# Optimization experiments

Measured on AMD Instinct MI355X. Metric: run time of the kernel, lower is better.

## Reference

```python
import jax, jax.numpy as jnp
import numpy as np

N_LAYERS = 2
D_MODEL = 1024
D_INNER = 2 * D_MODEL
D_STATE = 16
D_CONV = 4
DT_RANK = D_MODEL // 16  # 64
B_SZ, L = 1, 2048
EPS = 1e-5


def layernorm(x, w, b):
    mu = jnp.mean(x, axis=-1, keepdims=True)
    var = jnp.mean(jnp.square(x - mu), axis=-1, keepdims=True)
    return (x - mu) * jax.lax.rsqrt(var + EPS) * w + b


def mamba(x, in_w, cw, cb, xp_w, dtp_w, dtp_b, A_log, Dp, out_w):
    # x: [B, L, D_MODEL]
    Bn, Ln, _ = x.shape
    xz = jnp.einsum('bld,ed->ble', x, in_w)          # [B,L,2*D_INNER]
    xc, z = jnp.split(xz, 2, axis=-1)
    # causal depthwise conv1d (kernel D_CONV)
    xp = jnp.pad(xc, ((0, 0), (D_CONV - 1, 0), (0, 0)))
    xc = sum(xp[:, k:k + Ln, :] * cw[:, k] for k in range(D_CONV)) + cb
    xc = jax.nn.silu(xc)
    dbl = jnp.einsum('ble,re->blr', xc, xp_w)        # [B,L,DT_RANK+2*D_STATE]
    dt, Bm, Cm = jnp.split(dbl, [DT_RANK, DT_RANK + D_STATE], axis=-1)
    dt = jax.nn.softplus(jnp.einsum('blr,er->ble', dt, dtp_w) + dtp_b)  # [B,L,E]
    A = -jnp.exp(A_log)                              # [E,N], strictly negative
    dA = jnp.exp(dt[..., None] * A)                  # [B,L,E,N]
    dBu = (dt * xc)[..., None] * Bm[:, :, None, :]   # [B,L,E,N]

    def step(h, inp):
        dA_t, dBu_t, C_t = inp
        h = dA_t * h + dBu_t                         # [B,E,N]
        y = jnp.einsum('ben,bn->be', h, C_t)
        return h, y

    h0 = jnp.zeros((Bn, D_INNER, D_STATE), dA.dtype)
    _, ys = jax.lax.scan(step, h0, (dA.transpose(1, 0, 2, 3),
                                    dBu.transpose(1, 0, 2, 3),
                                    Cm.transpose(1, 0, 2)))
    y = ys.transpose(1, 0, 2) + xc * Dp              # [B,L,E]
    y = y * jax.nn.silu(z)
    return jnp.einsum('ble,de->bld', y, out_w)       # [B,L,D_MODEL]


def setup_inputs() -> dict:
    key = jax.random.key(0)
    ks = jax.random.split(key, 12)
    s = 0.02
    dt_init = np.log(np.expm1(0.01)).astype(np.float32)  # softplus^-1(0.01)
    A_row = jnp.log(jnp.arange(1, D_STATE + 1, dtype=jnp.float32))
    return {
        'x': jax.random.normal(ks[0], (B_SZ, L, D_MODEL), jnp.float32),
        'ln_w': jnp.ones((N_LAYERS, D_MODEL), jnp.float32),
        'ln_b': jnp.zeros((N_LAYERS, D_MODEL), jnp.float32),
        'in_proj_w': jax.random.normal(ks[1], (N_LAYERS, 2 * D_INNER, D_MODEL)) * s,
        'conv_w': jax.random.normal(ks[2], (N_LAYERS, D_INNER, D_CONV)) * 0.2,
        'conv_b': jnp.zeros((N_LAYERS, D_INNER), jnp.float32),
        'x_proj_w': jax.random.normal(ks[3], (N_LAYERS, DT_RANK + 2 * D_STATE, D_INNER)) * s,
        'dt_proj_w': jax.random.normal(ks[4], (N_LAYERS, D_INNER, DT_RANK)) * (DT_RANK ** -0.5),
        'dt_proj_b': jnp.full((N_LAYERS, D_INNER), dt_init),
        'A_log': jnp.broadcast_to(A_row, (N_LAYERS, D_INNER, D_STATE)).copy(),
        'D_skip': jnp.ones((N_LAYERS, D_INNER), jnp.float32),
        'out_proj_w': jax.random.normal(ks[5], (N_LAYERS, D_MODEL, D_INNER)) * s,
        'norm_f_w': jnp.ones((D_MODEL,), jnp.float32),
        'norm_f_b': jnp.zeros((D_MODEL,), jnp.float32),
    }


def reference(x, ln_w, ln_b, in_proj_w, conv_w, conv_b, x_proj_w, dt_proj_w,
              dt_proj_b, A_log, D_skip, out_proj_w, norm_f_w, norm_f_b):
    for i in range(N_LAYERS):
        h = layernorm(x, ln_w[i], ln_b[i])
        h = mamba(h, in_proj_w[i], conv_w[i], conv_b[i], x_proj_w[i],
                  dt_proj_w[i], dt_proj_b[i], A_log[i], D_skip[i], out_proj_w[i])
        x = h + x  # residual (dropout/drop_path are identity in eval)
    return layernorm(x, norm_f_w, norm_f_b)
```

## Files before the change

### kernel.cpp

```cpp
#include <hip/hip_runtime.h>
#include <hip/hip_bf16.h>
#include <math.h>

#define LSEQ 2048
#define DMODEL 1024
#define DINNER 2048
#define DSTATE 16
#define DCONV 4
#define DTRANK 64
#define RPROJ 96

#define CHUNK 32
#define NCHUNK (LSEQ / CHUNK)

typedef __attribute__((ext_vector_type(8))) short bf16x8;
typedef __attribute__((ext_vector_type(4))) float f32x4;

__device__ __forceinline__ float softplusf(float x) {
    return (x > 20.f) ? x : log1pf(__expf(x));
}
__device__ __forceinline__ float siluf(float x) {
    return x / (1.f + __expf(-x));
}
__device__ __forceinline__ short f2bf(float f) {
    union { float f; unsigned u; } v; v.f = f;
    unsigned r = v.u + 0x7FFFu + ((v.u >> 16) & 1u);
    return (short)(r >> 16);
}

__global__ __launch_bounds__(256) void cvt_bf16(
    const float* __restrict__ s, short* __restrict__ d, int n)
{
    const int i = (blockIdx.x * 256 + threadIdx.x) * 8;
    if (i >= n) return;
    const float4 a = *(const float4*)(s + i);
    const float4 b = *(const float4*)(s + i + 4);
    alignas(16) short h[8];
    h[0] = f2bf(a.x); h[1] = f2bf(a.y); h[2] = f2bf(a.z); h[3] = f2bf(a.w);
    h[4] = f2bf(b.x); h[5] = f2bf(b.y); h[6] = f2bf(b.z); h[7] = f2bf(b.w);
    *(uint4*)(d + i) = *(const uint4*)h;
}

__global__ __launch_bounds__(256) void ln_kernel(
    const float* __restrict__ x, const float* __restrict__ w,
    const float* __restrict__ b, float* __restrict__ outf,
    short* __restrict__ outb)
{
    __shared__ float s1[256], s2[256];
    const int row = blockIdx.x;
    const int tid = threadIdx.x;
    const float* xr = x + (size_t)row * DMODEL;
    float v[4];
    float s = 0.f, sq = 0.f;
#pragma unroll
    for (int k = 0; k < 4; k++) {
        v[k] = xr[k * 256 + tid];
        s += v[k];
        sq += v[k] * v[k];
    }
    s1[tid] = s; s2[tid] = sq;
    __syncthreads();
    for (int off = 128; off > 0; off >>= 1) {
        if (tid < off) { s1[tid] += s1[tid + off]; s2[tid] += s2[tid + off]; }
        __syncthreads();
    }
    const float mu = s1[0] * (1.f / DMODEL);
    const float var = s2[0] * (1.f / DMODEL) - mu * mu;
    const float rstd = rsqrtf(var + 1e-5f);
#pragma unroll
    for (int k = 0; k < 4; k++) {
        const int i = k * 256 + tid;
        const float o = (v[k] - mu) * rstd * w[i] + b[i];
        if (outf) outf[(size_t)row * DMODEL + i] = o;
        if (outb) outb[(size_t)row * DMODEL + i] = f2bf(o);
    }
}

template<int BN_T, int MODE>
__global__ __launch_bounds__(256) void gemm_mfma(
    const short* __restrict__ A,
    const short* __restrict__ W,
    float* __restrict__ C, int ldc,
    int M, int N, int K,
    const float* __restrict__ resid)
{
    constexpr int BK = 32;
    constexpr int HN = BN_T / 2;
    constexpr int NJ = BN_T / 32;
    constexpr int WISS = (BN_T * BK * 2) / 4096;
    __shared__ alignas(16) short As[128 * BK];
    __shared__ alignas(16) short Ws[BN_T * BK];

    const int tid = threadIdx.x;
    const int lane = tid & 63;
    const int w = tid >> 6;
    const int wr = w >> 1, wc = w & 1;
    const int row0 = blockIdx.y * 128;
    const int col0 = blockIdx.x * BN_T;

    const int srow = tid >> 2;
    const int skch = (tid & 3) * 8;

    f32x4 acc[4][NJ];
#pragma unroll
    for (int i = 0; i < 4; i++)
#pragma unroll
        for (int j = 0; j < NJ; j++) acc[i][j] = (f32x4)0.f;

    const int lrow = lane & 15;
    const int lk = (lane >> 4) * 8;

    for (int kt = 0; kt < K; kt += BK) {
        __syncthreads();
#pragma unroll
        for (int j = 0; j < 2; j++) {
            const short* gp = A + (size_t)(row0 + j * 64 + srow) * K + kt + skch;
            short* lp = As + j * 2048 + w * 512;
            __builtin_amdgcn_global_load_lds(
                (const __attribute__((address_space(1))) void*)gp,
                (__attribute__((address_space(3))) void*)lp, 16, 0, 0);
        }
#pragma unroll
        for (int j = 0; j < WISS; j++) {
            const int wrow = col0 + j * 64 + srow;
            const short* gp = W + (size_t)wrow * K + kt + skch;
            short* lp = Ws + j * 2048 + w * 512;
            if (wrow < N)
                __builtin_amdgcn_global_load_lds(
                    (const __attribute__((address_space(1))) void*)gp,
                    (__attribute__((address_space(3))) void*)lp, 16, 0, 0);
        }
        __syncthreads();

        bf16x8 af[4], bfr[NJ];
#pragma unroll
        for (int i = 0; i < 4; i++)
            af[i] = *(const bf16x8*)&As[(wr * 64 + i * 16 + lrow) * BK + lk];
#pragma unroll
        for (int j = 0; j < NJ; j++)
            bfr[j] = *(const bf16x8*)&Ws[(wc * HN + j * 16 + lrow) * BK + lk];
#pragma unroll
        for (int i = 0; i < 4; i++)
#pragma unroll
            for (int j = 0; j < NJ; j++)
                acc[i][j] = __builtin_amdgcn_mfma_f32_16x16x32_bf16(
                    af[i], bfr[j], acc[i][j], 0, 0, 0);
    }

    const int rbase = row0 + wr * 64;
    const int cbase = col0 + wc * HN;
#pragma unroll
    for (int i = 0; i < 4; i++) {
#pragma unroll
        for (int j = 0; j < NJ; j++) {
            const int gcol = cbase + j * 16 + lrow;
            if (gcol < N) {
#pragma unroll
                for (int r = 0; r < 4; r++) {
                    const int grow = rbase + i * 16 + (lane >> 4) * 4 + r;
                    float v = acc[i][j][r];
                    if (MODE == 2) v += resid[(size_t)grow * ldc + gcol];
                    C[(size_t)grow * ldc + gcol] = v;
                }
            }
        }
    }
}

#define BM 64
#define BN 64
#define BK16 16
__global__ __launch_bounds__(256) void gemm_nt(
    const float* __restrict__ A, int lda,
    const float* __restrict__ W, int ldw,
    float* __restrict__ C, int ldc,
    int M, int N, int K,
    const float* __restrict__ bias)
{
    __shared__ float As[BK16][BM];
    __shared__ float Ws[BK16][BN];
    const int tid = threadIdx.x;
    const int row0 = blockIdx.y * BM;
    const int col0 = blockIdx.x * BN;
    const int lr = tid >> 2;
    const int lk = (tid & 3) << 2;
    const int tx = tid & 15;
    const int ty = tid >> 4;

    float acc[4][4] = {{0.f}};

    for (int kt = 0; kt < K; kt += BK16) {
        const float4 av = *(const float4*)(A + (size_t)(row0 + lr) * lda + kt + lk);
        As[lk + 0][lr] = av.x; As[lk + 1][lr] = av.y;
        As[lk + 2][lr] = av.z; As[lk + 3][lr] = av.w;
        const float4 wv = *(const float4*)(W + (size_t)(col0 + lr) * ldw + kt + lk);
        Ws[lk + 0][lr] = wv.x; Ws[lk + 1][lr] = wv.y;
        Ws[lk + 2][lr] = wv.z; Ws[lk + 3][lr] = wv.w;
        __syncthreads();
#pragma unroll
        for (int k = 0; k < BK16; k++) {
            const float4 a4 = *(const float4*)&As[k][ty * 4];
            const float4 w4 = *(const float4*)&Ws[k][tx * 4];
            acc[0][0] += a4.x * w4.x; acc[0][1] += a4.x * w4.y;
            acc[0][2] += a4.x * w4.z; acc[0][3] += a4.x * w4.w;
            acc[1][0] += a4.y * w4.x; acc[1][1] += a4.y * w4.y;
            acc[1][2] += a4.y * w4.z; acc[1][3] += a4.y * w4.w;
            acc[2][0] += a4.z * w4.x; acc[2][1] += a4.z * w4.y;
            acc[2][2] += a4.z * w4.z; acc[2][3] += a4.z * w4.w;
            acc[3][0] += a4.w * w4.x; acc[3][1] += a4.w * w4.y;
            acc[3][2] += a4.w * w4.z; acc[3][3] += a4.w * w4.w;
        }
        __syncthreads();
    }

    const int c = col0 + tx * 4;
#pragma unroll
    for (int i = 0; i < 4; i++) {
        const int r = row0 + ty * 4 + i;
        float4 v = make_float4(acc[i][0], acc[i][1], acc[i][2], acc[i][3]);
        v.x = softplusf(v.x + bias[c + 0]);
        v.y = softplusf(v.y + bias[c + 1]);
        v.z = softplusf(v.z + bias[c + 2]);
        v.w = softplusf(v.w + bias[c + 3]);
        *(float4*)(C + (size_t)r * ldc + c) = v;
    }
}

__global__ __launch_bounds__(256) void conv_silu_kernel(
    const float* __restrict__ xz, const float* __restrict__ cw,
    const float* __restrict__ cb, float* __restrict__ xc,
    short* __restrict__ xcb)
{
    const int g = blockIdx.x * 256 + threadIdx.x;
    const int c = g & (DINNER - 1);
    const int t = g >> 11;
    float acc = cb[c];
#pragma unroll
    for (int k = 0; k < DCONV; k++) {
        const int tt = t - (DCONV - 1) + k;
        if (tt >= 0) acc += xz[(size_t)tt * (2 * DINNER) + c] * cw[c * DCONV + k];
    }
    const float o = siluf(acc);
    xc[(size_t)t * DINNER + c] = o;
    xcb[(size_t)t * DINNER + c] = f2bf(o);
}

__global__ __launch_bounds__(256) void scan_pass1(
    const float* __restrict__ dt,
    const float* __restrict__ xc,
    const float* __restrict__ dbl,
    const float* __restrict__ A_log,
    float* __restrict__ S,
    float* __restrict__ sumdt)
{
    const int e = blockIdx.x * 256 + threadIdx.x;
    const int c = blockIdx.y;
    float a[DSTATE];
#pragma unroll
    for (int n = 0; n < DSTATE; n++) a[n] = -__expf(A_log[(size_t)e * DSTATE + n]);
    float h[DSTATE];
#pragma unroll
    for (int n = 0; n < DSTATE; n++) h[n] = 0.f;
    float sd = 0.f;

    __shared__ float sBC[CHUNK][32];
    for (int i = threadIdx.x; i < CHUNK * 32; i += 256) {
        const int tl = i >> 5, j = i & 31;
        sBC[tl][j] = dbl[(size_t)(c * CHUNK + tl) * RPROJ + DTRANK + j];
    }
    __syncthreads();

    for (int tl = 0; tl < CHUNK; tl++) {
        const int t = c * CHUNK + tl;
        const float dtv = dt[(size_t)t * DINNER + e];
        const float du = dtv * xc[(size_t)t * DINNER + e];
        sd += dtv;
#pragma unroll
        for (int n = 0; n < DSTATE; n++) {
            const float dA = __expf(dtv * a[n]);
            h[n] = dA * h[n] + du * sBC[tl][n];
        }
    }
    sumdt[(size_t)c * DINNER + e] = sd;
#pragma unroll
    for (int n = 0; n < DSTATE; n++)
        S[((size_t)c * DSTATE + n) * DINNER + e] = h[n];
}

__global__ __launch_bounds__(256) void scan_pass2(
    const float* __restrict__ A_log,
    const float* __restrict__ sumdt,
    float* __restrict__ S)
{
    const int idx = blockIdx.x * 256 + threadIdx.x;
    const int e = idx & (DINNER - 1);
    const int n = idx >> 11;
    const float a = -__expf(A_log[(size_t)e * DSTATE + n]);
    float H = 0.f;
    for (int c = 0; c < NCHUNK; c++) {
        const size_t off = ((size_t)c * DSTATE + n) * DINNER + e;
        const float tmp = S[off];
        S[off] = H;
        const float P = __expf(a * sumdt[(size_t)c * DINNER + e]);
        H = P * H + tmp;
    }
}

__global__ __launch_bounds__(256) void scan_pass3(
    const float* __restrict__ dt,
    const float* __restrict__ xc,
    const float* __restrict__ dbl,
    const float* __restrict__ xz,
    const float* __restrict__ A_log,
    const float* __restrict__ Dp,
    const float* __restrict__ S,
    short* __restrict__ yb)
{
    const int e = blockIdx.x * 256 + threadIdx.x;
    const int c = blockIdx.y;
    float a[DSTATE];
#pragma unroll
    for (int n = 0; n < DSTATE; n++) a[n] = -__expf(A_log[(size_t)e * DSTATE + n]);
    float h[DSTATE];
#pragma unroll
    for (int n = 0; n < DSTATE; n++)
        h[n] = S[((size_t)c * DSTATE + n) * DINNER + e];
    const float dskip = Dp[e];

    __shared__ float sBC[CHUNK][32];
    for (int i = threadIdx.x; i < CHUNK * 32; i += 256) {
        const int tl = i >> 5, j = i & 31;
        sBC[tl][j] = dbl[(size_t)(c * CHUNK + tl) * RPROJ + DTRANK + j];
    }
    __syncthreads();

    for (int tl = 0; tl < CHUNK; tl++) {
        const int t = c * CHUNK + tl;
        const float dtv = dt[(size_t)t * DINNER + e];
        const float xcv = xc[(size_t)t * DINNER + e];
        const float du = dtv * xcv;
        float yv = 0.f;
#pragma unroll
        for (int n = 0; n < DSTATE; n++) {
            const float dA = __expf(dtv * a[n]);
            h[n] = dA * h[n] + du * sBC[tl][n];
            yv += h[n] * sBC[tl][16 + n];
        }
        const float zv = xz[(size_t)t * (2 * DINNER) + DINNER + e];
        yv = (yv + xcv * dskip) * siluf(zv);
        yb[(size_t)t * DINNER + e] = f2bf(yv);
    }
}

extern "C" void kernel_launch(void* const* d_in, const int* in_sizes, int n_in,
                              void* d_out, int out_size, void* d_ws, size_t ws_size,
                              hipStream_t stream) {
    const float* x_in   = (const float*)d_in[0];
    const float* ln_w   = (const float*)d_in[1];
    const float* ln_b   = (const float*)d_in[2];
    const float* in_w   = (const float*)d_in[3];
    const float* conv_w = (const float*)d_in[4];
    const float* conv_b = (const float*)d_in[5];
    const float* xp_w   = (const float*)d_in[6];
    const float* dtp_w  = (const float*)d_in[7];
    const float* dtp_b  = (const float*)d_in[8];
    const float* A_log  = (const float*)d_in[9];
    const float* D_skip = (const float*)d_in[10];
    const float* out_w  = (const float*)d_in[11];
    const float* nf_w   = (const float*)d_in[12];
    const float* nf_b   = (const float*)d_in[13];
    float* out = (float*)d_out;

    float* w = (float*)d_ws;
    float* buf_x = w; w += (size_t)LSEQ * DMODEL;
    float* xz    = w; w += (size_t)LSEQ * 2 * DINNER;
    float* xc    = w; w += (size_t)LSEQ * DINNER;
    float* dbl   = w; w += (size_t)LSEQ * RPROJ;
    float* dtb   = w; w += (size_t)LSEQ * DINNER;
    float* Sbuf  = w; w += (size_t)NCHUNK * DSTATE * DINNER;
    float* sumdt = w; w += (size_t)NCHUNK * DINNER;
    short* h_bf    = (short*)w; w += (size_t)LSEQ * DMODEL / 2;
    short* xc_bf   = (short*)w; w += (size_t)LSEQ * DINNER / 2;
    short* y_bf    = (short*)w; w += (size_t)LSEQ * DINNER / 2;
    short* in_w_bf  = (short*)w; w += (size_t)2 * (2 * DINNER) * DMODEL / 2;
    short* xp_w_bf  = (short*)w; w += (size_t)2 * RPROJ * DINNER / 2;
    short* out_w_bf = (short*)w; w += (size_t)2 * DMODEL * DINNER / 2;

    {
        const int n1 = 2 * (2 * DINNER) * DMODEL;
        cvt_bf16<<<dim3(n1 / (256 * 8)), dim3(256), 0, stream>>>(in_w, in_w_bf, n1);
        const int n2 = 2 * RPROJ * DINNER;
        cvt_bf16<<<dim3(n2 / (256 * 8)), dim3(256), 0, stream>>>(xp_w, xp_w_bf, n2);
        const int n3 = 2 * DMODEL * DINNER;
        cvt_bf16<<<dim3(n3 / (256 * 8)), dim3(256), 0, stream>>>(out_w, out_w_bf, n3);
    }

    for (int layer = 0; layer < 2; layer++) {
        const float* resid_src = (layer == 0) ? x_in : buf_x;
        ln_kernel<<<dim3(LSEQ), dim3(256), 0, stream>>>(
            resid_src, ln_w + layer * DMODEL, ln_b + layer * DMODEL,
            nullptr, h_bf);
        gemm_mfma<128, 0><<<dim3((2 * DINNER) / 128, LSEQ / 128), dim3(256), 0, stream>>>(
            h_bf, in_w_bf + (size_t)layer * 2 * DINNER * DMODEL,
            xz, 2 * DINNER, LSEQ, 2 * DINNER, DMODEL, nullptr);
        conv_silu_kernel<<<dim3((LSEQ * DINNER) / 256), dim3(256), 0, stream>>>(
            xz, conv_w + (size_t)layer * DINNER * DCONV, conv_b + layer * DINNER,
            xc, xc_bf);
        gemm_mfma<64, 0><<<dim3((RPROJ + 63) / 64, LSEQ / 128), dim3(256), 0, stream>>>(
            xc_bf, xp_w_bf + (size_t)layer * RPROJ * DINNER,
            dbl, RPROJ, LSEQ, RPROJ, DINNER, nullptr);
        gemm_nt<<<dim3(DINNER / BN, LSEQ / BM), dim3(256), 0, stream>>>(
            dbl, RPROJ, dtp_w + (size_t)layer * DINNER * DTRANK, DTRANK,
            dtb, DINNER, LSEQ, DINNER, DTRANK, dtp_b + layer * DINNER);
        const float* Al = A_log + (size_t)layer * DINNER * DSTATE;
        scan_pass1<<<dim3(DINNER / 256, NCHUNK), dim3(256), 0, stream>>>(
            dtb, xc, dbl, Al, Sbuf, sumdt);
        scan_pass2<<<dim3((DINNER * DSTATE) / 256), dim3(256), 0, stream>>>(
            Al, sumdt, Sbuf);
        scan_pass3<<<dim3(DINNER / 256, NCHUNK), dim3(256), 0, stream>>>(
            dtb, xc, dbl, xz, Al, D_skip + layer * DINNER, Sbuf, y_bf);
        gemm_mfma<64, 2><<<dim3(DMODEL / 64, LSEQ / 128), dim3(256), 0, stream>>>(
            y_bf, out_w_bf + (size_t)layer * DMODEL * DINNER,
            buf_x, DMODEL, LSEQ, DMODEL, DINNER, resid_src);
    }
    ln_kernel<<<dim3(LSEQ), dim3(256), 0, stream>>>(buf_x, nf_w, nf_b, out, nullptr);
}
```

Before: 530.1 us.

## Store xz and xc intermediates in bf16 and run dt_proj on MFMA

The in_proj GEMM now writes its output directly as bf16, and the fp32 xc buffer is removed. Conv, scan_pass1 and scan_pass3 read bf16 xz and xc and widen them to fp32. The fp32 SIMT dt_proj GEMM is replaced by the bf16 MFMA GEMM, which applies the fused bias and softplus in its epilogue, fed by a bf16 copy of dbl and dt_proj weights. The goal is to cut memory traffic on the large intermediates and speed up the dt projection, at the cost of reduced precision in dt, xc and z.

```diff
diff --git a/kernel.cpp b/kernel.cpp
--- a/kernel.cpp
+++ b/kernel.cpp
@@ -26,6 +26,11 @@
     union { float f; unsigned u; } v; v.f = f;
     unsigned r = v.u + 0x7FFFu + ((v.u >> 16) & 1u);
     return (short)(r >> 16);
+}
+__device__ __forceinline__ float bf2f(short h) {
+    union { unsigned u; float f; } v;
+    v.u = ((unsigned)(unsigned short)h) << 16;
+    return v.f;
 }
 
 __global__ __launch_bounds__(256) void cvt_bf16(
@@ -78,10 +83,11 @@
 
 template<int BN_T, int MODE>
 __global__ __launch_bounds__(256) void gemm_mfma(
-    const short* __restrict__ A,
-    const short* __restrict__ W,
-    float* __restrict__ C, int ldc,
+    const short* __restrict__ A, int lda,
+    const short* __restrict__ W, int ldw,
+    float* __restrict__ Cf, short* __restrict__ Cb, int ldc,
     int M, int N, int K,
+    const float* __restrict__ bias,
     const float* __restrict__ resid)
 {
     constexpr int BK = 32;
@@ -114,7 +120,7 @@
         __syncthreads();
 #pragma unroll
         for (int j = 0; j < 2; j++) {
-            const short* gp = A + (size_t)(row0 + j * 64 + srow) * K + kt + skch;
+            const short* gp = A + (size_t)(row0 + j * 64 + srow) * lda + kt + skch;
             short* lp = As + j * 2048 + w * 512;
             __builtin_amdgcn_global_load_lds(
                 (const __attribute__((address_space(1))) void*)gp,
@@ -123,7 +129,7 @@
 #pragma unroll
         for (int j = 0; j < WISS; j++) {
             const int wrow = col0 + j * 64 + srow;
-            const short* gp = W + (size_t)wrow * K + kt + skch;
+            const short* gp = W + (size_t)wrow * ldw + kt + skch;
             short* lp = Ws + j * 2048 + w * 512;
             if (wrow < N)
                 __builtin_amdgcn_global_load_lds(
@@ -159,77 +165,23 @@
                 for (int r = 0; r < 4; r++) {
                     const int grow = rbase + i * 16 + (lane >> 4) * 4 + r;
                     float v = acc[i][j][r];
+                    if (MODE == 1) v = softplusf(v + bias[gcol]);
                     if (MODE == 2) v += resid[(size_t)grow * ldc + gcol];
-                    C[(size_t)grow * ldc + gcol] = v;
+                    if (MODE == 3) {
+                        Cb[(size_t)grow * ldc + gcol] = f2bf(v);
+                    } else {
+                        Cf[(size_t)grow * ldc + gcol] = v;
+                        if (MODE == 4) Cb[(size_t)grow * ldc + gcol] = f2bf(v);
+                    }
                 }
             }
         }
     }
 }
 
-#define BM 64
-#define BN 64
-#define BK16 16
-__global__ __launch_bounds__(256) void gemm_nt(
-    const float* __restrict__ A, int lda,
-    const float* __restrict__ W, int ldw,
-    float* __restrict__ C, int ldc,
-    int M, int N, int K,
-    const float* __restrict__ bias)
-{
-    __shared__ float As[BK16][BM];
-    __shared__ float Ws[BK16][BN];
-    const int tid = threadIdx.x;
-    const int row0 = blockIdx.y * BM;
-    const int col0 = blockIdx.x * BN;
-    const int lr = tid >> 2;
-    const int lk = (tid & 3) << 2;
-    const int tx = tid & 15;
-    const int ty = tid >> 4;
-
-    float acc[4][4] = {{0.f}};
-
-    for (int kt = 0; kt < K; kt += BK16) {
-        const float4 av = *(const float4*)(A + (size_t)(row0 + lr) * lda + kt + lk);
-        As[lk + 0][lr] = av.x; As[lk + 1][lr] = av.y;
-        As[lk + 2][lr] = av.z; As[lk + 3][lr] = av.w;
-        const float4 wv = *(const float4*)(W + (size_t)(col0 + lr) * ldw + kt + lk);
-        Ws[lk + 0][lr] = wv.x; Ws[lk + 1][lr] = wv.y;
-        Ws[lk + 2][lr] = wv.z; Ws[lk + 3][lr] = wv.w;
-        __syncthreads();
-#pragma unroll
-        for (int k = 0; k < BK16; k++) {
-            const float4 a4 = *(const float4*)&As[k][ty * 4];
-            const float4 w4 = *(const float4*)&Ws[k][tx * 4];
-            acc[0][0] += a4.x * w4.x; acc[0][1] += a4.x * w4.y;
-            acc[0][2] += a4.x * w4.z; acc[0][3] += a4.x * w4.w;
-            acc[1][0] += a4.y * w4.x; acc[1][1] += a4.y * w4.y;
-            acc[1][2] += a4.y * w4.z; acc[1][3] += a4.y * w4.w;
-            acc[2][0] += a4.z * w4.x; acc[2][1] += a4.z * w4.y;
-            acc[2][2] += a4.z * w4.z; acc[2][3] += a4.z * w4.w;
-            acc[3][0] += a4.w * w4.x; acc[3][1] += a4.w * w4.y;
-            acc[3][2] += a4.w * w4.z; acc[3][3] += a4.w * w4.w;
-        }
-        __syncthreads();
-    }
-
-    const int c = col0 + tx * 4;
-#pragma unroll
-    for (int i = 0; i < 4; i++) {
-        const int r = row0 + ty * 4 + i;
-        float4 v = make_float4(acc[i][0], acc[i][1], acc[i][2], acc[i][3]);
-        v.x = softplusf(v.x + bias[c + 0]);
-        v.y = softplusf(v.y + bias[c + 1]);
-        v.z = softplusf(v.z + bias[c + 2]);
-        v.w = softplusf(v.w + bias[c + 3]);
-        *(float4*)(C + (size_t)r * ldc + c) = v;
-    }
-}
-
 __global__ __launch_bounds__(256) void conv_silu_kernel(
-    const float* __restrict__ xz, const float* __restrict__ cw,
-    const float* __restrict__ cb, float* __restrict__ xc,
-    short* __restrict__ xcb)
+    const short* __restrict__ xzb, const float* __restrict__ cw,
+    const float* __restrict__ cb, short* __restrict__ xcb)
 {
     const int g = blockIdx.x * 256 + threadIdx.x;
     const int c = g & (DINNER - 1);
@@ -238,16 +190,15 @@
 #pragma unroll
     for (int k = 0; k < DCONV; k++) {
         const int tt = t - (DCONV - 1) + k;
-        if (tt >= 0) acc += xz[(size_t)tt * (2 * DINNER) + c] * cw[c * DCONV + k];
-    }
-    const float o = siluf(acc);
-    xc[(size_t)t * DINNER + c] = o;
-    xcb[(size_t)t * DINNER + c] = f2bf(o);
+        if (tt >= 0)
+            acc += bf2f(xzb[(size_t)tt * (2 * DINNER) + c]) * cw[c * DCONV + k];
+    }
+    xcb[(size_t)t * DINNER + c] = f2bf(siluf(acc));
 }
 
 __global__ __launch_bounds__(256) void scan_pass1(
     const float* __restrict__ dt,
-    const float* __restrict__ xc,
+    const short* __restrict__ xcb,
     const float* __restrict__ dbl,
     const float* __restrict__ A_log,
     float* __restrict__ S,
@@ -273,7 +224,7 @@
     for (int tl = 0; tl < CHUNK; tl++) {
         const int t = c * CHUNK + tl;
         const float dtv = dt[(size_t)t * DINNER + e];
-        const float du = dtv * xc[(size_t)t * DINNER + e];
+        const float du = dtv * bf2f(xcb[(size_t)t * DINNER + e]);
         sd += dtv;
 #pragma unroll
         for (int n = 0; n < DSTATE; n++) {
@@ -308,9 +259,9 @@
 
 __global__ __launch_bounds__(256) void scan_pass3(
     const float* __restrict__ dt,
-    const float* __restrict__ xc,
+    const short* __restrict__ xcb,
     const float* __restrict__ dbl,
-    const float* __restrict__ xz,
+    const short* __restrict__ xzb,
     const float* __restrict__ A_log,
     const float* __restrict__ Dp,
     const float* __restrict__ S,
@@ -337,7 +288,7 @@
     for (int tl = 0; tl < CHUNK; tl++) {
         const int t = c * CHUNK + tl;
         const float dtv = dt[(size_t)t * DINNER + e];
-        const float xcv = xc[(size_t)t * DINNER + e];
+        const float xcv = bf2f(xcb[(size_t)t * DINNER + e]);
         const float du = dtv * xcv;
         float yv = 0.f;
 #pragma unroll
@@ -346,7 +297,7 @@
             h[n] = dA * h[n] + du * sBC[tl][n];
             yv += h[n] * sBC[tl][16 + n];
         }
-        const float zv = xz[(size_t)t * (2 * DINNER) + DINNER + e];
+        const float zv = bf2f(xzb[(size_t)t * (2 * DINNER) + DINNER + e]);
         yv = (yv + xcv * dskip) * siluf(zv);
         yb[(size_t)t * DINNER + e] = f2bf(yv);
     }
@@ -373,17 +324,18 @@
 
     float* w = (float*)d_ws;
     float* buf_x = w; w += (size_t)LSEQ * DMODEL;
-    float* xz    = w; w += (size_t)LSEQ * 2 * DINNER;
-    float* xc    = w; w += (size_t)LSEQ * DINNER;
     float* dbl   = w; w += (size_t)LSEQ * RPROJ;
     float* dtb   = w; w += (size_t)LSEQ * DINNER;
     float* Sbuf  = w; w += (size_t)NCHUNK * DSTATE * DINNER;
     float* sumdt = w; w += (size_t)NCHUNK * DINNER;
     short* h_bf    = (short*)w; w += (size_t)LSEQ * DMODEL / 2;
+    short* xz_bf   = (short*)w; w += (size_t)LSEQ * 2 * DINNER / 2;
     short* xc_bf   = (short*)w; w += (size_t)LSEQ * DINNER / 2;
     short* y_bf    = (short*)w; w += (size_t)LSEQ * DINNER / 2;
+    short* dbl_bf  = (short*)w; w += (size_t)LSEQ * RPROJ / 2 + 1;
     short* in_w_bf  = (short*)w; w += (size_t)2 * (2 * DINNER) * DMODEL / 2;
     short* xp_w_bf  = (short*)w; w += (size_t)2 * RPROJ * DINNER / 2;
+    short* dtp_w_bf = (short*)w; w += (size_t)2 * DINNER * DTRANK / 2;
     short* out_w_bf = (short*)w; w += (size_t)2 * DMODEL * DINNER / 2;
 
     {
@@ -393,6 +345,8 @@
         cvt_bf16<<<dim3(n2 / (256 * 8)), dim3(256), 0, stream>>>(xp_w, xp_w_bf, n2);
         const int n3 = 2 * DMODEL * DINNER;
         cvt_bf16<<<dim3(n3 / (256 * 8)), dim3(256), 0, stream>>>(out_w, out_w_bf, n3);
+        const int n4 = 2 * DINNER * DTRANK;
+        cvt_bf16<<<dim3(n4 / (256 * 8)), dim3(256), 0, stream>>>(dtp_w, dtp_w_bf, n4);
     }
 
     for (int layer = 0; layer < 2; layer++) {
@@ -400,28 +354,29 @@
         ln_kernel<<<dim3(LSEQ), dim3(256), 0, stream>>>(
             resid_src, ln_w + layer * DMODEL, ln_b + layer * DMODEL,
             nullptr, h_bf);
-        gemm_mfma<128, 0><<<dim3((2 * DINNER) / 128, LSEQ / 128), dim3(256), 0, stream>>>(
-            h_bf, in_w_bf + (size_t)layer * 2 * DINNER * DMODEL,
-            xz, 2 * DINNER, LSEQ, 2 * DINNER, DMODEL, nullptr);
+        gemm_mfma<128, 3><<<dim3((2 * DINNER) / 128, LSEQ / 128), dim3(256), 0, stream>>>(
+            h_bf, DMODEL, in_w_bf + (size_t)layer * 2 * DINNER * DMODEL, DMODEL,
+            nullptr, xz_bf, 2 * DINNER, LSEQ, 2 * DINNER, DMODEL, nullptr, nullptr);
         conv_silu_kernel<<<dim3((LSEQ * DINNER) / 256), dim3(256), 0, stream>>>(
-            xz, conv_w + (size_t)layer * DINNER * DCONV, conv_b + layer * DINNER,
-            xc, xc_bf);
-        gemm_mfma<64, 0><<<dim3((RPROJ + 63) / 64, LSEQ / 128), dim3(256), 0, stream>>>(
-            xc_bf, xp_w_bf + (size_t)layer * RPROJ * DINNER,
-            dbl, RPROJ, LSEQ, RPROJ, DINNER, nullptr);
-        gemm_nt<<<dim3(DINNER / BN, LSEQ / BM), dim3(256), 0, stream>>>(
-            dbl, RPROJ, dtp_w + (size_t)layer * DINNER * DTRANK, DTRANK,
-            dtb, DINNER, LSEQ, DINNER, DTRANK, dtp_b + layer * DINNER);
+            xz_bf, conv_w + (size_t)layer * DINNER * DCONV, conv_b + layer * DINNER,
+            xc_bf);
+        gemm_mfma<64, 4><<<dim3((RPROJ + 63) / 64, LSEQ / 128), dim3(256), 0, stream>>>(
+            xc_bf, DINNER, xp_w_bf + (size_t)layer * RPROJ * DINNER, DINNER,
+            dbl, dbl_bf, RPROJ, LSEQ, RPROJ, DINNER, nullptr, nullptr);
+        gemm_mfma<128, 1><<<dim3(DINNER / 128, LSEQ / 128), dim3(256), 0, stream>>>(
+            dbl_bf, RPROJ, dtp_w_bf + (size_t)layer * DINNER * DTRANK, DTRANK,
+            dtb, nullptr, DINNER, LSEQ, DINNER, DTRANK,
+            dtp_b + layer * DINNER, nullptr);
         const float* Al = A_log + (size_t)layer * DINNER * DSTATE;
         scan_pass1<<<dim3(DINNER / 256, NCHUNK), dim3(256), 0, stream>>>(
-            dtb, xc, dbl, Al, Sbuf, sumdt);
+            dtb, xc_bf, dbl, Al, Sbuf, sumdt);
         scan_pass2<<<dim3((DINNER * DSTATE) / 256), dim3(256), 0, stream>>>(
             Al, sumdt, Sbuf);
         scan_pass3<<<dim3(DINNER / 256, NCHUNK), dim3(256), 0, stream>>>(
-            dtb, xc, dbl, xz, Al, D_skip + layer * DINNER, Sbuf, y_bf);
+            dtb, xc_bf, dbl, xz_bf, Al, D_skip + layer * DINNER, Sbuf, y_bf);
         gemm_mfma<64, 2><<<dim3(DMODEL / 64, LSEQ / 128), dim3(256), 0, stream>>>(
-            y_bf, out_w_bf + (size_t)layer * DMODEL * DINNER,
-            buf_x, DMODEL, LSEQ, DMODEL, DINNER, resid_src);
+            y_bf, DINNER, out_w_bf + (size_t)layer * DMODEL * DINNER, DINNER,
+            buf_x, nullptr, DMODEL, LSEQ, DMODEL, DINNER, nullptr, resid_src);
     }
     ln_kernel<<<dim3(LSEQ), dim3(256), 0, stream>>>(buf_x, nf_w, nf_b, out, nullptr);
 }
```

Measured after the change: 574.2 us. 1.08x slower.
